# Kernel tuning notes

Measured on AMD Instinct MI355X. Metric: run time of the kernel, lower is better.

Reference implementation:

```python
import jax, jax.numpy as jnp
import numpy as np

V = 128   # vocab_size
H = 1024  # rnn_hidden_size
L = 2     # rnn_num_layers
B = 64    # batch
T = 256   # seq_len


def setup_inputs() -> dict:
    key = jax.random.key(0)
    ks = jax.random.split(key, 1 + 4 * L)
    inp = {"x": jax.random.randint(ks[0], (B, T), 0, V)}
    s = 1.0 / np.sqrt(H)  # torch GRU init range
    k = 1
    for l in range(L):
        in_dim = V if l == 0 else 2 * H
        inp[f"Wih{l}"] = jax.random.uniform(ks[k], (2, 3 * H, in_dim), minval=-s, maxval=s); k += 1
        inp[f"Whh{l}"] = jax.random.uniform(ks[k], (2, 3 * H, H), minval=-s, maxval=s); k += 1
        inp[f"bih{l}"] = jax.random.uniform(ks[k], (2, 3 * H), minval=-s, maxval=s); k += 1
        inp[f"bhh{l}"] = jax.random.uniform(ks[k], (2, 3 * H), minval=-s, maxval=s); k += 1
    return inp


def _gru_dir(x_seq, Wih, Whh, bih, bhh, reverse):
    # x_seq: [B, T, in_dim]; Wih: [3H, in_dim]; Whh: [3H, H]
    xp = jnp.einsum('bti,gi->btg', x_seq, Wih) + bih  # batched input projection
    if reverse:
        xp = xp[:, ::-1]
    h0 = jnp.zeros((x_seq.shape[0], H), x_seq.dtype)

    def step(h, xpt):
        g = h @ Whh.T + bhh
        xr, xz, xn = jnp.split(xpt, 3, axis=-1)
        hr, hz, hn = jnp.split(g, 3, axis=-1)
        r = jax.nn.sigmoid(xr + hr)
        z = jax.nn.sigmoid(xz + hz)
        n = jnp.tanh(xn + r * hn)
        h_new = (1.0 - z) * n + z * h
        return h_new, h_new

    hT, ys = jax.lax.scan(step, h0, jnp.swapaxes(xp, 0, 1))  # scan over time
    ys = jnp.swapaxes(ys, 0, 1)  # [B, T, H]
    if reverse:
        ys = ys[:, ::-1]
    return ys, hT


def _encoder(x, params):
    inp_seq = jax.nn.one_hot(x, V, dtype=jnp.float32)  # [B, T, V]
    hiddens = []
    for (Wih, Whh, bih, bhh) in params:
        yf, hf = _gru_dir(inp_seq, Wih[0], Whh[0], bih[0], bhh[0], False)
        yb, hb = _gru_dir(inp_seq, Wih[1], Whh[1], bih[1], bhh[1], True)
        inp_seq = jnp.concatenate([yf, yb], axis=-1)  # [B, T, 2H]
        hiddens += [hf, hb]
    return inp_seq, jnp.stack(hiddens)  # ([B,T,2H], [2L,B,H])


def reference(x, Wih0, Whh0, bih0, bhh0, Wih1, Whh1, bih1, bhh1):
    params = [(Wih0, Whh0, bih0, bhh0), (Wih1, Whh1, bih1, bhh1)]
    return _encoder(x, params)
```

## Files before the change

kernel.cpp:

```cpp
#include <hip/hip_runtime.h>
#include <stdint.h>
#include <math.h>


#define B_  64
#define T_  256
#define H_  1024
#define G3_ 3072

#define SW_BYTES (3 * 32 * 64 * 16)
#define SX_ROW 132
#define SMEM_BYTES (SW_BYTES + 48 * SX_ROW * 4)

typedef __attribute__((ext_vector_type(8))) __bf16 bf16x8;
typedef __attribute__((ext_vector_type(4))) float  f32x4;

union FragU { uint4 u; bf16x8 b; };

__device__ __forceinline__ float bf2f(unsigned short v) {
  return __builtin_bit_cast(float, (uint32_t)v << 16);
}
__device__ __forceinline__ unsigned short f2bf(float f) {
  uint32_t u = __builtin_bit_cast(uint32_t, f);
  u += 0x7FFFu + ((u >> 16) & 1u);
  return (unsigned short)(u >> 16);
}

__device__ __forceinline__ void bar_fast(unsigned* cnt, unsigned& target) {
  asm volatile("s_waitcnt vmcnt(0)" ::: "memory");
  __syncthreads();
  if (threadIdx.x == 0) {
    __hip_atomic_fetch_add(cnt, 1u, __ATOMIC_RELAXED, __HIP_MEMORY_SCOPE_AGENT);
    unsigned spins = 0;
    while (__hip_atomic_load(cnt, __ATOMIC_RELAXED, __HIP_MEMORY_SCOPE_AGENT) < target) {
      __builtin_amdgcn_s_sleep(2);
      if (++spins > (1u << 22)) break;
    }
  }
  __syncthreads();
  target += 64;
}

__device__ __forceinline__ void bar_fenced(unsigned* cnt, unsigned& target) {
  __syncthreads();
  if (threadIdx.x == 0) {
    __builtin_amdgcn_fence(__ATOMIC_RELEASE, "agent");
    __hip_atomic_fetch_add(cnt, 1u, __ATOMIC_RELAXED, __HIP_MEMORY_SCOPE_AGENT);
    unsigned spins = 0;
    while (__hip_atomic_load(cnt, __ATOMIC_RELAXED, __HIP_MEMORY_SCOPE_AGENT) < target) {
      __builtin_amdgcn_s_sleep(8);
      if (++spins > (1u << 20)) break;
    }
    __builtin_amdgcn_fence(__ATOMIC_ACQUIRE, "agent");
  }
  __syncthreads();
  target += 64;
}

__global__ void detect_dtype(const unsigned short* __restrict__ p, int* __restrict__ flag) {
  const int i = threadIdx.x;
  const unsigned short v = p[2 * i];
  const int e = (v >> 7) & 0xFF;
  const unsigned long long m = __ballot(e <= 124);
  if (i == 0) *flag = (m == ~0ull) ? 1 : 0;
}

__device__ __forceinline__ float load_canon(const void* src, int i, bool isbf) {
  return isbf ? bf2f(((const unsigned short*)src)[i]) : ((const float*)src)[i];
}

__global__ void prep_split(const void* __restrict__ src, int n,
                           unsigned short* __restrict__ hi, unsigned short* __restrict__ lo,
                           const int* __restrict__ flag) {
  const int i = blockIdx.x * blockDim.x + threadIdx.x;
  if (i >= n) return;
  const bool isbf = (*flag != 0);
  const float f = load_canon(src, i, isbf);
  const unsigned short h = f2bf(f);
  hi[i] = h;
  lo[i] = f2bf(f - bf2f(h));
}

__global__ void prep_f32(const void* __restrict__ src, int n,
                         float* __restrict__ dst, const int* __restrict__ flag) {
  const int i = blockIdx.x * blockDim.x + threadIdx.x;
  if (i >= n) return;
  const bool isbf = (*flag != 0);
  dst[i] = load_canon(src, i, isbf);
}

#define LD2(K, OFF)                                                         \
  asm volatile("global_load_dwordx4 %0, %2, off offset:" OFF " sc0 sc1\n\t" \
               "global_load_dwordx4 %1, %3, off offset:" OFF " sc0 sc1"     \
               : "=&v"(ah[K].u), "=&v"(al[K].u)                             \
               : "v"(aph), "v"(apl));

#define STH(P, V)                                                 \
  asm volatile("global_store_short %0, %1, off sc0 sc1"           \
               :: "v"(P), "v"(V) : "memory");

template<int LAYER>
__global__ __launch_bounds__(256, 1) void gru_scan(
    const int*            __restrict__ x,
    const float*          __restrict__ Wih0f,
    const float*          __restrict__ bihf,
    const _Float16*       __restrict__ xp1,
    const unsigned short* __restrict__ WhhH,
    const unsigned short* __restrict__ WhhL,
    const float*          __restrict__ bhhf,
    unsigned short*       __restrict__ hhi,
    unsigned short*       __restrict__ hlo,
    unsigned short*       __restrict__ ys0_hi,
    unsigned short*       __restrict__ ys0_lo,
    void*                 __restrict__ d_out,
    const int*            __restrict__ flag,
    unsigned*             __restrict__ bar_mem)
{
  extern __shared__ unsigned char smem[];
  unsigned short* sW = (unsigned short*)smem;
  float*          sX = (float*)(smem + SW_BYTES);

  const int j0   = blockIdx.x << 4;
  const int d    = blockIdx.y;
  const int tid  = threadIdx.x;
  const int w    = tid >> 6;
  const int lane = tid & 63;
  const int quad = lane >> 4, l15 = lane & 15;
  const bool out_bf = (*flag != 0);
  const bool wlo    = (*flag == 0);

  const int j = j0 + l15;
  const size_t HF_HALF = (size_t)2 * B_ * H_;

  {
    const unsigned short* base = WhhH + (size_t)d * G3_ * H_;
    for (int idx = tid; idx < 48 * 128; idx += 256) {
      const int row = idx >> 7;
      const int c16 = idx & 127;
      const int g = row >> 4, u = row & 15;
      const int kt = c16 >> 2, q = c16 & 3;
      const uint4 v = *(const uint4*)(base + (size_t)(g * H_ + j0 + u) * H_ + (c16 << 3));
      *(uint4*)&sW[(((g << 5) + kt) << 9) + (((q << 4) + u) << 3)] = v;
    }
  }
  if (LAYER == 0) {
    const float* W0 = Wih0f + (size_t)d * G3_ * 128;
    for (int idx = tid; idx < 48 * 32; idx += 256) {
      const int row = idx >> 5, c = (idx & 31) << 2;
      const int g = row >> 4, u = row & 15;
      const float4 v = *(const float4*)(W0 + (size_t)(g * H_ + j0 + u) * 128 + c);
      *(float4*)&sX[row * SX_ROW + c] = v;
    }
  }
  __syncthreads();

  const int am = (w << 4) + l15;
  const unsigned short *aphS[2], *aplS[2];
  unsigned short *hhiS[2], *hloS[2];
#pragma unroll
  for (int s = 0; s < 2; ++s) {
    aphS[s] = hhi + s * HF_HALF + ((size_t)d * B_ + am) * H_ + (quad << 3);
    aplS[s] = hlo + s * HF_HALF + ((size_t)d * B_ + am) * H_ + (quad << 3);
    hhiS[s] = hhi + s * HF_HALF + (size_t)d * B_ * H_;
    hloS[s] = hlo + s * HF_HALF + (size_t)d * B_ * H_;
  }

  const unsigned short* bplG[3];
#pragma unroll
  for (int g = 0; g < 3; ++g)
    bplG[g] = WhhL + (size_t)d * G3_ * H_ + (size_t)(g * H_ + j) * H_ + (quad << 3);

  const size_t dj = (size_t)d * G3_ + j;
  const float bhr = bhhf[dj];
  const float bhz = bhhf[dj + H_];
  const float bhn = bhhf[dj + 2 * H_];
  float bir = 0.f, biz = 0.f, bin_ = 0.f;
  const float *sXr = nullptr, *sXz = nullptr, *sXn = nullptr;
  if (LAYER == 0) {
    bir  = bihf[dj];
    biz  = bihf[dj + H_];
    bin_ = bihf[dj + 2 * H_];
    sXr = sX + (size_t)l15 * SX_ROW;
    sXz = sX + (size_t)(16 + l15) * SX_ROW;
    sXn = sX + (size_t)(32 + l15) * SX_ROW;
  }
  const _Float16* xpd = (LAYER == 1) ? (xp1 + (size_t)d * (B_ * T_) * G3_) : nullptr;

  float*          out_f  = (float*)d_out;
  unsigned short* out_b  = (unsigned short*)d_out;
  const size_t    HIDOFF = (size_t)B_ * T_ * 2048;

  unsigned* cnt = bar_mem + (size_t)d * 256;
  unsigned target = 64;
  const int bb = (w << 4) + (quad << 2);
  float hprev[4] = {0.f, 0.f, 0.f, 0.f};

  if (!wlo) {
    float xr[4], xz[4], xn[4];
    _Float16 xph[12];
    {
      const int te = d ? (T_ - 1) : 0;
      if (LAYER == 0) {
#pragma unroll
        for (int r = 0; r < 4; ++r) {
          const int tok = x[(bb + r) * T_ + te];
          xr[r] = sXr[tok] + bir; xz[r] = sXz[tok] + biz; xn[r] = sXn[tok] + bin_;
        }
      } else {
#pragma unroll
        for (int r = 0; r < 4; ++r) {
          const _Float16* xpb = xpd + ((size_t)(bb + r) * T_ + te) * G3_;
          xph[r * 3 + 0] = xpb[j]; xph[r * 3 + 1] = xpb[j + H_]; xph[r * 3 + 2] = xpb[j + 2 * H_];
        }
      }
    }

    for (int t = 0; t < T_; ++t) {
      const int t_eff = d ? (T_ - 1 - t) : t;
      const int pi = t & 1, po = pi ^ 1;
      const unsigned short* aph = aphS[pi];
      const unsigned short* apl = aplS[pi];

      FragU ah[32], al[32];
      LD2(0, "0")    LD2(1, "64")   LD2(2, "128")  LD2(3, "192")
      LD2(4, "256")  LD2(5, "320")  LD2(6, "384")  LD2(7, "448")
      LD2(8, "512")  LD2(9, "576")  LD2(10, "640") LD2(11, "704")
      LD2(12, "768") LD2(13, "832") LD2(14, "896") LD2(15, "960")
      LD2(16, "1024") LD2(17, "1088") LD2(18, "1152") LD2(19, "1216")
      LD2(20, "1280") LD2(21, "1344") LD2(22, "1408") LD2(23, "1472")
      LD2(24, "1536") LD2(25, "1600") LD2(26, "1664") LD2(27, "1728")
      LD2(28, "1792") LD2(29, "1856") LD2(30, "1920") LD2(31, "1984")

      f32x4 acc[3] = {};
      asm volatile("s_waitcnt vmcnt(32)" ::: "memory");
      __builtin_amdgcn_sched_barrier(0);
#pragma unroll
      for (int kt = 0; kt < 16; ++kt) {
        FragU f0, f1, f2;
        f0.u = *(const uint4*)(sW + ((kt      ) << 9) + (lane << 3));
        f1.u = *(const uint4*)(sW + ((kt +  32) << 9) + (lane << 3));
        f2.u = *(const uint4*)(sW + ((kt +  64) << 9) + (lane << 3));
        acc[0] = __builtin_amdgcn_mfma_f32_16x16x32_bf16(ah[kt].b, f0.b, acc[0], 0, 0, 0);
        acc[0] = __builtin_amdgcn_mfma_f32_16x16x32_bf16(al[kt].b, f0.b, acc[0], 0, 0, 0);
        acc[1] = __builtin_amdgcn_mfma_f32_16x16x32_bf16(ah[kt].b, f1.b, acc[1], 0, 0, 0);
        acc[1] = __builtin_amdgcn_mfma_f32_16x16x32_bf16(al[kt].b, f1.b, acc[1], 0, 0, 0);
        acc[2] = __builtin_amdgcn_mfma_f32_16x16x32_bf16(ah[kt].b, f2.b, acc[2], 0, 0, 0);
        acc[2] = __builtin_amdgcn_mfma_f32_16x16x32_bf16(al[kt].b, f2.b, acc[2], 0, 0, 0);
      }
      asm volatile("s_waitcnt vmcnt(0)" ::: "memory");
      __builtin_amdgcn_sched_barrier(0);
#pragma unroll
      for (int kt = 16; kt < 32; ++kt) {
        FragU f0, f1, f2;
        f0.u = *(const uint4*)(sW + ((kt      ) << 9) + (lane << 3));
        f1.u = *(const uint4*)(sW + ((kt +  32) << 9) + (lane << 3));
        f2.u = *(const uint4*)(sW + ((kt +  64) << 9) + (lane << 3));
        acc[0] = __builtin_amdgcn_mfma_f32_16x16x32_bf16(ah[kt].b, f0.b, acc[0], 0, 0, 0);
        acc[0] = __builtin_amdgcn_mfma_f32_16x16x32_bf16(al[kt].b, f0.b, acc[0], 0, 0, 0);
        acc[1] = __builtin_amdgcn_mfma_f32_16x16x32_bf16(ah[kt].b, f1.b, acc[1], 0, 0, 0);
        acc[1] = __builtin_amdgcn_mfma_f32_16x16x32_bf16(al[kt].b, f1.b, acc[1], 0, 0, 0);
        acc[2] = __builtin_amdgcn_mfma_f32_16x16x32_bf16(ah[kt].b, f2.b, acc[2], 0, 0, 0);
        acc[2] = __builtin_amdgcn_mfma_f32_16x16x32_bf16(al[kt].b, f2.b, acc[2], 0, 0, 0);
      }

      if (LAYER == 1) {
#pragma unroll
        for (int r = 0; r < 4; ++r) {
          xr[r] = (float)xph[r * 3 + 0];
          xz[r] = (float)xph[r * 3 + 1];
          xn[r] = (float)xph[r * 3 + 2];
        }
      }

      unsigned short* pHi = hhiS[po] + (size_t)bb * H_ + j;
      unsigned short* pLo = hloS[po] + (size_t)bb * H_ + j;
#pragma unroll
      for (int r = 0; r < 4; ++r) {
        const int b = bb + r;
        const float gr = acc[0][r] + bhr;
        const float gz = acc[1][r] + bhz;
        const float gn = acc[2][r] + bhn;
        const float rg = 1.f / (1.f + expf(-(xr[r] + gr)));
        const float zg = 1.f / (1.f + expf(-(xz[r] + gz)));
        const float ng = tanhf(xn[r] + rg * gn);
        const float hnew = (1.f - zg) * ng + zg * hprev[r];
        hprev[r] = hnew;

        const unsigned short hi = f2bf(hnew);
        const unsigned short lo = f2bf(hnew - bf2f(hi));
        STH(pHi + (size_t)r * H_, (uint32_t)hi);
        STH(pLo + (size_t)r * H_, (uint32_t)lo);

        const size_t yoff = ((size_t)b * T_ + t_eff) * 2048 + d * H_ + j;
        if (LAYER == 0) {
          ys0_hi[yoff] = hi;
          ys0_lo[yoff] = lo;
        } else {
          if (out_bf) out_b[yoff] = hi; else out_f[yoff] = hnew;
        }
        if (t == T_ - 1) {
          const size_t hh = HIDOFF + ((size_t)(LAYER * 2 + d) * B_ + b) * H_ + j;
          if (out_bf) out_b[hh] = hi; else out_f[hh] = hnew;
        }
      }

      if (t + 1 < T_) {
        const int te = d ? (T_ - 2 - t) : (t + 1);
        if (LAYER == 0) {
#pragma unroll
          for (int r = 0; r < 4; ++r) {
            const int tok = x[(bb + r) * T_ + te];
            xr[r] = sXr[tok] + bir; xz[r] = sXz[tok] + biz; xn[r] = sXn[tok] + bin_;
          }
        } else {
#pragma unroll
          for (int r = 0; r < 4; ++r) {
            const _Float16* xpb = xpd + ((size_t)(bb + r) * T_ + te) * G3_;
            xph[r * 3 + 0] = xpb[j]; xph[r * 3 + 1] = xpb[j + H_]; xph[r * 3 + 2] = xpb[j + 2 * H_];
          }
        }
        bar_fast(cnt, target);
      }
    }
  } else {
    for (int t = 0; t < T_; ++t) {
      const int t_eff = d ? (T_ - 1 - t) : t;
      const int pi = t & 1, po = pi ^ 1;

      float xr[4], xz[4], xn[4];
      if (LAYER == 0) {
#pragma unroll
        for (int r = 0; r < 4; ++r) {
          const int tok = x[(bb + r) * T_ + t_eff];
          xr[r] = sXr[tok] + bir; xz[r] = sXz[tok] + biz; xn[r] = sXn[tok] + bin_;
        }
      } else {
#pragma unroll
        for (int r = 0; r < 4; ++r) {
          const _Float16* xpb = xpd + ((size_t)(bb + r) * T_ + t_eff) * G3_;
          xr[r] = (float)xpb[j]; xz[r] = (float)xpb[j + H_]; xn[r] = (float)xpb[j + 2 * H_];
        }
      }

      const unsigned short* aph = aphS[pi];
      const unsigned short* apl = aplS[pi];
      f32x4 acc[3] = {};
#pragma unroll
      for (int kt = 0; kt < 32; ++kt) {
        FragU ah, al;
        ah.u = *(const uint4*)(aph + (kt << 5));
        al.u = *(const uint4*)(apl + (kt << 5));
#pragma unroll
        for (int g = 0; g < 3; ++g) {
          FragU fb, fl;
          fb.u = *(const uint4*)(sW + (((g << 5) + kt) << 9) + (lane << 3));
          fl.u = *(const uint4*)(bplG[g] + (kt << 5));
          acc[g] = __builtin_amdgcn_mfma_f32_16x16x32_bf16(ah.b, fb.b, acc[g], 0, 0, 0);
          acc[g] = __builtin_amdgcn_mfma_f32_16x16x32_bf16(al.b, fb.b, acc[g], 0, 0, 0);
          acc[g] = __builtin_amdgcn_mfma_f32_16x16x32_bf16(ah.b, fl.b, acc[g], 0, 0, 0);
        }
      }

#pragma unroll
      for (int r = 0; r < 4; ++r) {
        const int b = bb + r;
        const float gr = acc[0][r] + bhr;
        const float gz = acc[1][r] + bhz;
        const float gn = acc[2][r] + bhn;
        const float rg = 1.f / (1.f + expf(-(xr[r] + gr)));
        const float zg = 1.f / (1.f + expf(-(xz[r] + gz)));
        const float ng = tanhf(xn[r] + rg * gn);
        const float hnew = (1.f - zg) * ng + zg * hprev[r];
        hprev[r] = hnew;

        const size_t ho = (size_t)b * H_ + j;
        const unsigned short hi = f2bf(hnew);
        const unsigned short lo = f2bf(hnew - bf2f(hi));
        hhiS[po][ho] = hi;
        hloS[po][ho] = lo;

        const size_t yoff = ((size_t)b * T_ + t_eff) * 2048 + d * H_ + j;
        if (LAYER == 0) {
          ys0_hi[yoff] = hi;
          ys0_lo[yoff] = lo;
        } else {
          if (out_bf) out_b[yoff] = hi; else out_f[yoff] = hnew;
        }
        if (t == T_ - 1) {
          const size_t hh = HIDOFF + ((size_t)(LAYER * 2 + d) * B_ + b) * H_ + j;
          if (out_bf) out_b[hh] = hi; else out_f[hh] = hnew;
        }
      }

      if (t + 1 < T_) bar_fenced(cnt, target);
    }
  }
}

__global__ __launch_bounds__(256) void xp1_gemm(
    const unsigned short* __restrict__ Ahi,
    const unsigned short* __restrict__ Alo,
    const unsigned short* __restrict__ Bhi,
    const unsigned short* __restrict__ Blo,
    const float*          __restrict__ biasf,
    _Float16*             __restrict__ xp1,
    const int*            __restrict__ flag)
{
  const int nt  = blockIdx.x;
  const int mt  = blockIdx.y;
  const int d   = blockIdx.z;
  const int tid = threadIdx.x;
  const int w = tid >> 6, lane = tid & 63;
  const int quad = lane >> 4, l15 = lane & 15;
  const int wm = w >> 1, wn = w & 1;
  const bool wlo = (*flag == 0);

  __shared__ unsigned short sAh[128][40];
  __shared__ unsigned short sAl[128][40];
  __shared__ unsigned short sBh[128][40];
  __shared__ unsigned short sBl[128][40];

  const int srow = tid >> 1;
  const int scol = (tid & 1) << 4;
  const unsigned short* gAh = Ahi + (size_t)(mt * 128 + srow) * 2048 + scol;
  const unsigned short* gAl = Alo + (size_t)(mt * 128 + srow) * 2048 + scol;
  const unsigned short* gBh = Bhi + (size_t)d * G3_ * 2048
                                  + (size_t)(nt * 128 + srow) * 2048 + scol;
  const unsigned short* gBl = Blo + (size_t)d * G3_ * 2048
                                  + (size_t)(nt * 128 + srow) * 2048 + scol;

  f32x4 acc[4][4] = {};

  for (int k0 = 0; k0 < 2048; k0 += 32) {
    const uint4 a0 = *(const uint4*)(gAh + k0);
    const uint4 a1 = *(const uint4*)(gAh + k0 + 8);
    const uint4 l0 = *(const uint4*)(gAl + k0);
    const uint4 l1 = *(const uint4*)(gAl + k0 + 8);
    const uint4 b0 = *(const uint4*)(gBh + k0);
    const uint4 b1 = *(const uint4*)(gBh + k0 + 8);
    uint4 c0, c1;
    if (wlo) { c0 = *(const uint4*)(gBl + k0); c1 = *(const uint4*)(gBl + k0 + 8); }
    __syncthreads();
    *(uint4*)&sAh[srow][scol]     = a0;
    *(uint4*)&sAh[srow][scol + 8] = a1;
    *(uint4*)&sAl[srow][scol]     = l0;
    *(uint4*)&sAl[srow][scol + 8] = l1;
    *(uint4*)&sBh[srow][scol]     = b0;
    *(uint4*)&sBh[srow][scol + 8] = b1;
    if (wlo) {
      *(uint4*)&sBl[srow][scol]     = c0;
      *(uint4*)&sBl[srow][scol + 8] = c1;
    }
    __syncthreads();

    bf16x8 fah[4], fal[4], fbh[4];
#pragma unroll
    for (int i = 0; i < 4; ++i) {
      FragU fa; fa.u = *(const uint4*)&sAh[(wm << 6) + (i << 4) + l15][quad << 3]; fah[i] = fa.b;
      FragU fl; fl.u = *(const uint4*)&sAl[(wm << 6) + (i << 4) + l15][quad << 3]; fal[i] = fl.b;
      FragU fb; fb.u = *(const uint4*)&sBh[(wn << 6) + (i << 4) + l15][quad << 3]; fbh[i] = fb.b;
    }
#pragma unroll
    for (int i = 0; i < 4; ++i)
#pragma unroll
      for (int jj = 0; jj < 4; ++jj) {
        acc[i][jj] = __builtin_amdgcn_mfma_f32_16x16x32_bf16(fah[i], fbh[jj], acc[i][jj], 0, 0, 0);
        acc[i][jj] = __builtin_amdgcn_mfma_f32_16x16x32_bf16(fal[i], fbh[jj], acc[i][jj], 0, 0, 0);
      }
    if (wlo) {
#pragma unroll
      for (int jj = 0; jj < 4; ++jj) {
        FragU fc; fc.u = *(const uint4*)&sBl[(wn << 6) + (jj << 4) + l15][quad << 3];
#pragma unroll
        for (int i = 0; i < 4; ++i)
          acc[i][jj] = __builtin_amdgcn_mfma_f32_16x16x32_bf16(fah[i], fc.b, acc[i][jj], 0, 0, 0);
      }
    }
  }

#pragma unroll
  for (int jj = 0; jj < 4; ++jj) {
    const int col = nt * 128 + (wn << 6) + (jj << 4) + l15;
    const float bias = biasf[(size_t)d * G3_ + col];
#pragma unroll
    for (int i = 0; i < 4; ++i) {
      const int m = mt * 128 + (wm << 6) + (i << 4) + (quad << 2);
      _Float16* op = xp1 + ((size_t)d * (B_ * T_) + m) * G3_ + col;
#pragma unroll
      for (int r = 0; r < 4; ++r) op[(size_t)r * G3_] = (_Float16)(acc[i][jj][r] + bias);
    }
  }
}

extern "C" void kernel_launch(void* const* d_in, const int* in_sizes, int n_in,
                              void* d_out, int out_size, void* d_ws, size_t ws_size,
                              hipStream_t stream)
{
  const int*  x    = (const int*)d_in[0];
  const void* Wih0 = d_in[1];
  const void* Whh0 = d_in[2];
  const void* bih0 = d_in[3];
  const void* bhh0 = d_in[4];
  const void* Wih1 = d_in[5];
  const void* Whh1 = d_in[6];
  const void* bih1 = d_in[7];
  const void* bhh1 = d_in[8];

  const size_t FLAG_B = 256;
  const size_t XP1_B  = (size_t)2 * B_ * T_ * G3_ * 2;
  const size_t YS_B   = (size_t)B_ * T_ * 2048 * 2;
  const size_t WHH_B  = (size_t)2 * G3_ * H_ * 2;
  const size_t WIH1_B = (size_t)2 * G3_ * 2048 * 2;
  const size_t WIH0_B = (size_t)2 * G3_ * 128 * 4;
  const size_t BIAS_B = (size_t)2 * G3_ * 4;
  const size_t HB_B   = (size_t)2 * 2 * B_ * H_ * 2;
  const size_t BAR_B  = 4096;
  const size_t NEED = FLAG_B + XP1_B + 2 * YS_B + 4 * WHH_B + 2 * WIH1_B
                    + WIH0_B + 4 * BIAS_B + 2 * HB_B + BAR_B;
  if (ws_size < NEED) return;

  char* p = (char*)d_ws;
  int*            flag    = (int*)p;            p += FLAG_B;
  _Float16*       xp1     = (_Float16*)p;       p += XP1_B;
  unsigned short* ys0_hi  = (unsigned short*)p; p += YS_B;
  unsigned short* ys0_lo  = (unsigned short*)p; p += YS_B;
  unsigned short* Whh0H   = (unsigned short*)p; p += WHH_B;
  unsigned short* Whh0L   = (unsigned short*)p; p += WHH_B;
  unsigned short* Whh1H   = (unsigned short*)p; p += WHH_B;
  unsigned short* Whh1L   = (unsigned short*)p; p += WHH_B;
  unsigned short* Wih1H   = (unsigned short*)p; p += WIH1_B;
  unsigned short* Wih1L   = (unsigned short*)p; p += WIH1_B;
  float*          Wih0f   = (float*)p;          p += WIH0_B;
  float*          bih0f   = (float*)p;          p += BIAS_B;
  float*          bhh0f   = (float*)p;          p += BIAS_B;
  float*          bih1f   = (float*)p;          p += BIAS_B;
  float*          bhh1f   = (float*)p;          p += BIAS_B;
  char*           hbase   = p;
  unsigned short* hhi     = (unsigned short*)hbase;
  unsigned short* hlo     = (unsigned short*)(hbase + HB_B);
  unsigned*       bar     = (unsigned*)(hbase + 2 * HB_B);

  hipFuncSetAttribute((const void*)&gru_scan<0>,
                      hipFuncAttributeMaxDynamicSharedMemorySize, SMEM_BYTES);
  hipFuncSetAttribute((const void*)&gru_scan<1>,
                      hipFuncAttributeMaxDynamicSharedMemorySize, SMEM_BYTES);

  detect_dtype<<<1, 64, 0, stream>>>((const unsigned short*)bih0, flag);

  const int NWHH  = 2 * G3_ * H_;
  const int NWIH1 = 2 * G3_ * 2048;
  const int NWIH0 = 2 * G3_ * 128;
  const int NBIAS = 2 * G3_;
  prep_split<<<(NWHH  + 255) / 256, 256, 0, stream>>>(Whh0, NWHH,  Whh0H, Whh0L, flag);
  prep_split<<<(NWHH  + 255) / 256, 256, 0, stream>>>(Whh1, NWHH,  Whh1H, Whh1L, flag);
  prep_split<<<(NWIH1 + 255) / 256, 256, 0, stream>>>(Wih1, NWIH1, Wih1H, Wih1L, flag);
  prep_f32<<<(NWIH0 + 255) / 256, 256, 0, stream>>>(Wih0, NWIH0, Wih0f, flag);
  prep_f32<<<(NBIAS + 255) / 256, 256, 0, stream>>>(bih0, NBIAS, bih0f, flag);
  prep_f32<<<(NBIAS + 255) / 256, 256, 0, stream>>>(bhh0, NBIAS, bhh0f, flag);
  prep_f32<<<(NBIAS + 255) / 256, 256, 0, stream>>>(bih1, NBIAS, bih1f, flag);
  prep_f32<<<(NBIAS + 255) / 256, 256, 0, stream>>>(bhh1, NBIAS, bhh1f, flag);

  hipMemsetAsync(hbase, 0, 2 * HB_B + BAR_B, stream);
  gru_scan<0><<<dim3(64, 2), 256, SMEM_BYTES, stream>>>(
      x, Wih0f, bih0f, nullptr, Whh0H, Whh0L, bhh0f,
      hhi, hlo, ys0_hi, ys0_lo, d_out, flag, bar);

  xp1_gemm<<<dim3(24, 128, 2), 256, 0, stream>>>(ys0_hi, ys0_lo, Wih1H, Wih1L, bih1f, xp1, flag);

  hipMemsetAsync(hbase, 0, 2 * HB_B + BAR_B, stream);
  gru_scan<1><<<dim3(64, 2), 256, SMEM_BYTES, stream>>>(
      x, nullptr, nullptr, xp1, Whh1H, Whh1L, bhh1f,
      hhi, hlo, nullptr, nullptr, d_out, flag, bar);
}
```

Baseline: 11.00 ms.

## Split GRU scan batch across blocks and use hierarchical grid barrier

The persistent GRU scan grid is doubled by splitting the batch across a new z dimension, so each block runs 128 threads over 32 batch rows. The flat counter barrier is replaced by a two-level barrier: sub-counters per group of 8 block indices, a root counter, and a release flag that waiters poll. The sigmoid and tanh calls are swapped for clamped __expf approximations. This is meant to spread per-step work over more CUs and cut atomic contention on one counter, at the cost of loading each Whh slice into shared memory twice and running a more involved barrier.

Result: slower. 12.49 ms (+13.5%).

```diff
diff --git a/kernel.cpp b/kernel.cpp
--- a/kernel.cpp
+++ b/kernel.cpp
@@ -26,35 +26,34 @@
   return (unsigned short)(u >> 16);
 }
 
-__device__ __forceinline__ void bar_fast(unsigned* cnt, unsigned& target) {
-  asm volatile("s_waitcnt vmcnt(0)" ::: "memory");
-  __syncthreads();
-  if (threadIdx.x == 0) {
-    __hip_atomic_fetch_add(cnt, 1u, __ATOMIC_RELAXED, __HIP_MEMORY_SCOPE_AGENT);
+__device__ __forceinline__ float sigm_fast(float x) {
+  x = fminf(fmaxf(x, -60.f), 60.f);
+  return 1.f / (1.f + __expf(-x));
+}
+__device__ __forceinline__ float tanh_fast(float x) {
+  const float xc = fminf(fmaxf(x, -15.f), 15.f);
+  const float e = __expf(2.f * xc);
+  return (e - 1.f) / (e + 1.f);
+}
+
+__device__ __forceinline__ void bar_arrive_wait(unsigned* bar, unsigned k) {
+  unsigned* sub = bar + 32u * (1u + (blockIdx.x & 7u));
+  bool rel = false;
+  if (__hip_atomic_fetch_add(sub, 1u, __ATOMIC_RELAXED, __HIP_MEMORY_SCOPE_AGENT)
+      == 16u * k - 1u) {
+    if (__hip_atomic_fetch_add(bar, 1u, __ATOMIC_RELAXED, __HIP_MEMORY_SCOPE_AGENT)
+        == 8u * k - 1u) {
+      __hip_atomic_store(bar + 384, k, __ATOMIC_RELAXED, __HIP_MEMORY_SCOPE_AGENT);
+      rel = true;
+    }
+  }
+  if (!rel) {
     unsigned spins = 0;
-    while (__hip_atomic_load(cnt, __ATOMIC_RELAXED, __HIP_MEMORY_SCOPE_AGENT) < target) {
-      __builtin_amdgcn_s_sleep(2);
-      if (++spins > (1u << 22)) break;
-    }
-  }
-  __syncthreads();
-  target += 64;
-}
-
-__device__ __forceinline__ void bar_fenced(unsigned* cnt, unsigned& target) {
-  __syncthreads();
-  if (threadIdx.x == 0) {
-    __builtin_amdgcn_fence(__ATOMIC_RELEASE, "agent");
-    __hip_atomic_fetch_add(cnt, 1u, __ATOMIC_RELAXED, __HIP_MEMORY_SCOPE_AGENT);
-    unsigned spins = 0;
-    while (__hip_atomic_load(cnt, __ATOMIC_RELAXED, __HIP_MEMORY_SCOPE_AGENT) < target) {
-      __builtin_amdgcn_s_sleep(8);
+    while (__hip_atomic_load(bar + 384, __ATOMIC_RELAXED, __HIP_MEMORY_SCOPE_AGENT) < k) {
+      __builtin_amdgcn_s_sleep(4);
       if (++spins > (1u << 20)) break;
     }
-    __builtin_amdgcn_fence(__ATOMIC_ACQUIRE, "agent");
-  }
-  __syncthreads();
-  target += 64;
+  }
 }
 
 __global__ void detect_dtype(const unsigned short* __restrict__ p, int* __restrict__ flag) {
@@ -100,7 +99,7 @@
                :: "v"(P), "v"(V) : "memory");
 
 template<int LAYER>
-__global__ __launch_bounds__(256, 1) void gru_scan(
+__global__ __launch_bounds__(128, 1) void gru_scan(
     const int*            __restrict__ x,
     const float*          __restrict__ Wih0f,
     const float*          __restrict__ bihf,
@@ -122,6 +121,7 @@
 
   const int j0   = blockIdx.x << 4;
   const int d    = blockIdx.y;
+  const int bh   = blockIdx.z;
   const int tid  = threadIdx.x;
   const int w    = tid >> 6;
   const int lane = tid & 63;
@@ -134,7 +134,7 @@
 
   {
     const unsigned short* base = WhhH + (size_t)d * G3_ * H_;
-    for (int idx = tid; idx < 48 * 128; idx += 256) {
+    for (int idx = tid; idx < 48 * 128; idx += 128) {
       const int row = idx >> 7;
       const int c16 = idx & 127;
       const int g = row >> 4, u = row & 15;
@@ -145,7 +145,7 @@
   }
   if (LAYER == 0) {
     const float* W0 = Wih0f + (size_t)d * G3_ * 128;
-    for (int idx = tid; idx < 48 * 32; idx += 256) {
+    for (int idx = tid; idx < 48 * 32; idx += 128) {
       const int row = idx >> 5, c = (idx & 31) << 2;
       const int g = row >> 4, u = row & 15;
       const float4 v = *(const float4*)(W0 + (size_t)(g * H_ + j0 + u) * 128 + c);
@@ -154,7 +154,8 @@
   }
   __syncthreads();
 
-  const int am = (w << 4) + l15;
+  const int am = (bh << 5) + (w << 4) + l15;
+  const int bb = (bh << 5) + (w << 4) + (quad << 2);
   const unsigned short *aphS[2], *aplS[2];
   unsigned short *hhiS[2], *hloS[2];
 #pragma unroll
@@ -190,9 +191,7 @@
   unsigned short* out_b  = (unsigned short*)d_out;
   const size_t    HIDOFF = (size_t)B_ * T_ * 2048;
 
-  unsigned* cnt = bar_mem + (size_t)d * 256;
-  unsigned target = 64;
-  const int bb = (w << 4) + (quad << 2);
+  unsigned* bar = bar_mem + (size_t)d * 1024;
   float hprev[4] = {0.f, 0.f, 0.f, 0.f};
 
   if (!wlo) {
@@ -280,9 +279,9 @@
         const float gr = acc[0][r] + bhr;
         const float gz = acc[1][r] + bhz;
         const float gn = acc[2][r] + bhn;
-        const float rg = 1.f / (1.f + expf(-(xr[r] + gr)));
-        const float zg = 1.f / (1.f + expf(-(xz[r] + gz)));
-        const float ng = tanhf(xn[r] + rg * gn);
+        const float rg = sigm_fast(xr[r] + gr);
+        const float zg = sigm_fast(xz[r] + gz);
+        const float ng = tanh_fast(xn[r] + rg * gn);
         const float hnew = (1.f - zg) * ng + zg * hprev[r];
         hprev[r] = hnew;
 
@@ -305,6 +304,8 @@
       }
 
       if (t + 1 < T_) {
+        asm volatile("s_waitcnt vmcnt(0)" ::: "memory");
+        __syncthreads();
         const int te = d ? (T_ - 2 - t) : (t + 1);
         if (LAYER == 0) {
 #pragma unroll
@@ -319,7 +320,8 @@
             xph[r * 3 + 0] = xpb[j]; xph[r * 3 + 1] = xpb[j + H_]; xph[r * 3 + 2] = xpb[j + 2 * H_];
           }
         }
-        bar_fast(cnt, target);
+        if (tid == 0) bar_arrive_wait(bar, (unsigned)(t + 1));
+        __syncthreads();
       }
     }
   } else {
@@ -392,7 +394,15 @@
         }
       }
 
-      if (t + 1 < T_) bar_fenced(cnt, target);
+      if (t + 1 < T_) {
+        __syncthreads();
+        if (tid == 0) {
+          __builtin_amdgcn_fence(__ATOMIC_RELEASE, "agent");
+          bar_arrive_wait(bar, (unsigned)(t + 1));
+          __builtin_amdgcn_fence(__ATOMIC_ACQUIRE, "agent");
+        }
+        __syncthreads();
+      }
     }
   }
 }
@@ -514,7 +524,7 @@
   const size_t WIH0_B = (size_t)2 * G3_ * 128 * 4;
   const size_t BIAS_B = (size_t)2 * G3_ * 4;
   const size_t HB_B   = (size_t)2 * 2 * B_ * H_ * 2;
-  const size_t BAR_B  = 4096;
+  const size_t BAR_B  = 8192;
   const size_t NEED = FLAG_B + XP1_B + 2 * YS_B + 4 * WHH_B + 2 * WIH1_B
                     + WIH0_B + 4 * BIAS_B + 2 * HB_B + BAR_B;
   if (ws_size < NEED) return;
@@ -561,14 +571,14 @@
   prep_f32<<<(NBIAS + 255) / 256, 256, 0, stream>>>(bhh1, NBIAS, bhh1f, flag);
 
   hipMemsetAsync(hbase, 0, 2 * HB_B + BAR_B, stream);
-  gru_scan<0><<<dim3(64, 2), 256, SMEM_BYTES, stream>>>(
+  gru_scan<0><<<dim3(64, 2, 2), 128, SMEM_BYTES, stream>>>(
       x, Wih0f, bih0f, nullptr, Whh0H, Whh0L, bhh0f,
       hhi, hlo, ys0_hi, ys0_lo, d_out, flag, bar);
 
   xp1_gemm<<<dim3(24, 128, 2), 256, 0, stream>>>(ys0_hi, ys0_lo, Wih1H, Wih1L, bih1f, xp1, flag);
 
   hipMemsetAsync(hbase, 0, 2 * HB_B + BAR_B, stream);
-  gru_scan<1><<<dim3(64, 2), 256, SMEM_BYTES, stream>>>(
+  gru_scan<1><<<dim3(64, 2, 2), 128, SMEM_BYTES, stream>>>(
       x, nullptr, nullptr, xp1, Whh1H, Whh1L, bhh1f,
       hhi, hlo, nullptr, nullptr, d_out, flag, bar);
 }
```
